# Kernel tuning notes

Hardware: AMD Instinct MI355X
Metric: run time of the kernel (lower is better)

The kernel has to match this reference:

```python
import jax, jax.numpy as jnp
import numpy as np

D_CONV = 4
D_STATE = 16
DT_RANK = 64


def _silu(x):
    return x * jax.nn.sigmoid(x)


def setup_inputs() -> dict:
    key = jax.random.key(0)
    ks = jax.random.split(key, 10)
    B, L, dim = 2, 1024, 1024
    d_inner = 2 * dim
    s = lambda fan: 1.0 / np.sqrt(fan)
    inp = {
        "x": jax.random.normal(ks[0], (B, L, dim), jnp.float32),
        "ln_w": jnp.ones((dim,), jnp.float32),
        "ln_b": jnp.zeros((dim,), jnp.float32),
        "w_in": jax.random.normal(ks[1], (2 * d_inner, dim), jnp.float32) * s(dim),
        "conv_w": jax.random.normal(ks[2], (d_inner, D_CONV), jnp.float32) * s(D_CONV),
        "conv_b": jnp.zeros((d_inner,), jnp.float32),
        "w_xproj": jax.random.normal(ks[3], (DT_RANK + 2 * D_STATE, d_inner), jnp.float32) * s(d_inner),
        "w_dt": jax.random.normal(ks[4], (d_inner, DT_RANK), jnp.float32) * s(DT_RANK),
        "b_dt": jax.random.normal(ks[5], (d_inner,), jnp.float32) * 0.1,
        # S4D-real init: A = -(1..d_state) per channel
        "a_log": jnp.tile(jnp.log(jnp.arange(1, D_STATE + 1, dtype=jnp.float32)), (d_inner, 1)),
        "d_skip": jnp.ones((d_inner,), jnp.float32),
        "w_out": jax.random.normal(ks[6], (dim, d_inner), jnp.float32) * s(d_inner),
    }
    return inp


def reference(x, ln_w, ln_b, w_in, conv_w, conv_b, w_xproj, w_dt, b_dt, a_log, d_skip, w_out):
    B, L, dim = x.shape
    residual = x

    # LayerNorm
    mu = jnp.mean(x, axis=-1, keepdims=True)
    var = jnp.mean((x - mu) ** 2, axis=-1, keepdims=True)
    xn = (x - mu) * jax.lax.rsqrt(var + 1e-5) * ln_w + ln_b

    # in_proj -> (x_ssm, z) each (B, L, d_inner)
    xz = jnp.einsum("bld,ed->ble", xn, w_in)
    d_inner = xz.shape[-1] // 2
    xs, z = xz[..., :d_inner], xz[..., d_inner:]

    # depthwise causal conv1d (kernel D_CONV) + SiLU
    xp = jnp.pad(xs, ((0, 0), (D_CONV - 1, 0), (0, 0)))
    xc = conv_b
    for k in range(D_CONV):
        xc = xc + conv_w[:, k] * xp[:, k : k + L, :]
    u = _silu(xc)  # (B, L, d_inner)

    # x_proj -> dt, B, C
    x_dbl = jnp.einsum("ble,re->blr", u, w_xproj)
    dt_r = x_dbl[..., :DT_RANK]
    B_ssm = x_dbl[..., DT_RANK : DT_RANK + D_STATE]         # (B, L, n)
    C_ssm = x_dbl[..., DT_RANK + D_STATE :]                 # (B, L, n)

    dt = jax.nn.softplus(jnp.einsum("blr,er->ble", dt_r, w_dt) + b_dt)  # (B, L, d_inner)

    A = -jnp.exp(a_log)  # (d_inner, n)
    deltaA = jnp.exp(jnp.einsum("ble,en->blen", dt, A))            # (B, L, e, n)
    deltaBu = jnp.einsum("ble,bln,ble->blen", dt, B_ssm, u)        # (B, L, e, n)

    # selective scan over L
    def step(h, ins):
        dA_t, dBu_t, C_t = ins
        h = dA_t * h + dBu_t                       # (B, e, n)
        y = jnp.einsum("ben,bn->be", h, C_t)
        return h, y

    h0 = jnp.zeros((B, d_inner, D_STATE), xs.dtype)
    _, ys = jax.lax.scan(
        step,
        h0,
        (deltaA.transpose(1, 0, 2, 3), deltaBu.transpose(1, 0, 2, 3), C_ssm.transpose(1, 0, 2)),
    )
    y = ys.transpose(1, 0, 2) + u * d_skip         # (B, L, e)

    y = y * _silu(z)
    out = jnp.einsum("ble,de->bld", y, w_out)
    return residual + out
```

## Files before the change

kernel.cpp:

```cpp
#include <hip/hip_runtime.h>
#include <hip/hip_bf16.h>


#define LC 32
#define NCHUNK 32

typedef short bf16x8 __attribute__((ext_vector_type(8)));
typedef float f32x4  __attribute__((ext_vector_type(4)));

static __device__ __forceinline__ float siluf(float x) { return x / (1.f + __expf(-x)); }
static __device__ __forceinline__ unsigned short f2bf(float f) {
    unsigned int u = __float_as_uint(f);
    unsigned int r = (u + 0x7fffu + ((u >> 16) & 1u)) >> 16;
    return (unsigned short)r;
}
static __device__ __forceinline__ float bfb(unsigned short u) {
    return __uint_as_float(((unsigned int)u) << 16);
}
static __device__ __forceinline__ void gload_lds16(const void* g, void* l) {
    __builtin_amdgcn_global_load_lds(
        (const __attribute__((address_space(1))) void*)g,
        (__attribute__((address_space(3))) void*)l, 16, 0, 0);
}

__global__ __launch_bounds__(256) void setup_kernel(
    const float* __restrict__ w_in,  unsigned short* __restrict__ w_in_b,
    const float* __restrict__ w_out, unsigned short* __restrict__ w_out_b,
    const float* __restrict__ w_dt,  unsigned short* __restrict__ w_dt_b,
    const float* __restrict__ x,
    const float* __restrict__ ln_w,
    const float* __restrict__ ln_b,
    unsigned short* __restrict__ xn)
{
    int bid = blockIdx.x, tid = threadIdx.x;
    if (bid < 6272) {
        int i = bid * 256 + tid;
        const float* in; unsigned short* outp; int j;
        if (i < 1048576)      { in = w_in;  outp = w_in_b;  j = i; }
        else if (i < 1572864) { in = w_out; outp = w_out_b; j = i - 1048576; }
        else if (i < 1605632) { in = w_dt;  outp = w_dt_b;  j = i - 1572864; }
        else return;
        float4 v = reinterpret_cast<const float4*>(in)[j];
        ushort4 o = { f2bf(v.x), f2bf(v.y), f2bf(v.z), f2bf(v.w) };
        reinterpret_cast<ushort4*>(outp)[j] = o;
        return;
    }
    int m = bid - 6272;
    const float4* xr = reinterpret_cast<const float4*>(x) + (size_t)m * 256;
    float4 r = xr[tid];
    float f0 = r.x, f1 = r.y, f2 = r.z, f3 = r.w;
    float s  = f0 + f1 + f2 + f3;
    float s2 = f0*f0 + f1*f1 + f2*f2 + f3*f3;
    #pragma unroll
    for (int off = 32; off > 0; off >>= 1) {
        s  += __shfl_down(s, off);
        s2 += __shfl_down(s2, off);
    }
    __shared__ float red[8];
    if ((tid & 63) == 0) { red[tid >> 6] = s; red[4 + (tid >> 6)] = s2; }
    __syncthreads();
    float st = red[0] + red[1] + red[2] + red[3];
    float qt = red[4] + red[5] + red[6] + red[7];
    float mu   = st * (1.f / 1024.f);
    float var  = qt * (1.f / 1024.f) - mu * mu;
    float rstd = rsqrtf(var + 1e-5f);
    float4 wv = reinterpret_cast<const float4*>(ln_w)[tid];
    float4 bv = reinterpret_cast<const float4*>(ln_b)[tid];
    ushort4 o = { f2bf((f0 - mu) * rstd * wv.x + bv.x),
                  f2bf((f1 - mu) * rstd * wv.y + bv.y),
                  f2bf((f2 - mu) * rstd * wv.z + bv.z),
                  f2bf((f3 - mu) * rstd * wv.w + bv.w) };
    reinterpret_cast<ushort4*>(xn + (size_t)m * 1024)[tid] = o;
}

__global__ __launch_bounds__(256) void gemm_bf16_nt(
    const unsigned short* __restrict__ A, int lda,
    const unsigned short* __restrict__ B, int ldb,
    int Kslice,
    float* __restrict__ C, unsigned short* __restrict__ Cb, int ldc,
    int ep, size_t Cstride)
{
    __shared__ short As[3 * 64 * 32];
    __shared__ short Bs[3 * 128 * 32];
    int tid = threadIdx.x;
    int z = blockIdx.z;
    A += (size_t)z * Kslice;
    B += (size_t)z * Kslice;
    C += (size_t)z * Cstride;

    int gx = gridDim.x;
    int wg = blockIdx.y * gx + blockIdx.x;
    int nwg = gx * gridDim.y;
    int cpx = nwg >> 3;
    int swz = (wg & 7) * cpx + (wg >> 3);
    int bx = swz % gx, by = swz / gx;

    int m0 = by * 64, n0 = bx * 128;
    int lane = tid & 63, wave = tid >> 6;
    int wm = (wave >> 1) * 32, wn = (wave & 1) * 64;
    int frow = lane & 15, fq = lane >> 4;

    f32x4 acc[2][4] = {};

    int lrow = lane >> 2;
    int scol = (lane & 3) * 8;
    const unsigned short* AgL = A + (size_t)(m0 + wave * 16 + lrow) * lda + scol;
    const unsigned short* BgL = B + (size_t)(n0 + wave * 16 + lrow) * ldb + scol;
    int aoff = (wave * 16) * 32;
    int boff = (wave * 16) * 32;

    #pragma unroll
    for (int p = 0; p < 2; ++p) {
        int nk = p * 32;
        gload_lds16(AgL + nk,                    As + p * 2048 + aoff);
        gload_lds16(BgL + nk,                    Bs + p * 4096 + boff);
        gload_lds16(BgL + (size_t)64 * ldb + nk, Bs + p * 4096 + boff + 64 * 32);
    }

    int cur = 0;
    for (int k0 = 0; k0 < Kslice; k0 += 32) {
        if (k0 + 32 < Kslice) {
            asm volatile("s_waitcnt vmcnt(3) lgkmcnt(0)" ::: "memory");
        } else {
            asm volatile("s_waitcnt vmcnt(0) lgkmcnt(0)" ::: "memory");
        }
        __builtin_amdgcn_s_barrier();
        int nk = k0 + 64;
        if (nk < Kslice) {
            int stg = cur - 1; if (stg < 0) stg = 2;
            gload_lds16(AgL + nk,                    As + stg * 2048 + aoff);
            gload_lds16(BgL + nk,                    Bs + stg * 4096 + boff);
            gload_lds16(BgL + (size_t)64 * ldb + nk, Bs + stg * 4096 + boff + 64 * 32);
        }
        const short* Ac = As + cur * 2048;
        const short* Bc = Bs + cur * 4096;
        bf16x8 af[2], bfr[4];
        #pragma unroll
        for (int i = 0; i < 2; ++i)
            af[i] = *reinterpret_cast<const bf16x8*>(Ac + (wm + i * 16 + frow) * 32 + fq * 8);
        #pragma unroll
        for (int j = 0; j < 4; ++j)
            bfr[j] = *reinterpret_cast<const bf16x8*>(Bc + (wn + j * 16 + frow) * 32 + fq * 8);
        #pragma unroll
        for (int i = 0; i < 2; ++i)
            #pragma unroll
            for (int j = 0; j < 4; ++j)
                acc[i][j] = __builtin_amdgcn_mfma_f32_16x16x32_bf16(af[i], bfr[j], acc[i][j], 0, 0, 0);
        cur = (cur == 2) ? 0 : cur + 1;
    }

    int cn = lane & 15, rq = (lane >> 4) * 4;
    #pragma unroll
    for (int i = 0; i < 2; ++i) {
        #pragma unroll
        for (int j = 0; j < 4; ++j) {
            #pragma unroll
            for (int r = 0; r < 4; ++r) {
                int row = m0 + wm + i * 16 + rq + r;
                int col = n0 + wn + j * 16 + cn;
                float v = acc[i][j][r];
                if (ep == 0) {
                    C[(size_t)row * ldc + col] = v;
                } else {
                    Cb[(size_t)row * ldc + col] = f2bf(v);
                }
            }
        }
    }
}

__global__ __launch_bounds__(256) void out_reduce(
    const float* __restrict__ part, const float* __restrict__ x,
    float* __restrict__ out)
{
    int i = blockIdx.x * 256 + threadIdx.x;
    float4 s = reinterpret_cast<const float4*>(x)[i];
    #pragma unroll
    for (int z = 0; z < 4; ++z) {
        float4 p = reinterpret_cast<const float4*>(part + (size_t)z * 2097152)[i];
        s.x += p.x; s.y += p.y; s.z += p.z; s.w += p.w;
    }
    reinterpret_cast<float4*>(out)[i] = s;
}

__global__ __launch_bounds__(256) void xproj_splitk(
    const unsigned short* __restrict__ xz,
    const float* __restrict__ cw,
    const float* __restrict__ cb,
    const float* __restrict__ B,
    unsigned short* __restrict__ u,
    float* __restrict__ part)
{
    __shared__ float As[16][68];
    __shared__ float Bs[16][100];
    int tid = threadIdx.x;
    int m0 = blockIdx.x * 64;
    int k0 = blockIdx.y * 64;
    int tx = tid & 15;
    int ty = tid >> 4;
    float acc[4][6] = {};
    int arow = tid >> 2, akg = (tid & 3) << 2;
    int brow1 = (256 + tid) >> 2, bkg1 = ((256 + tid) & 3) << 2;
    int m = m0 + arow;
    int l = m & 1023;

    for (int ks = 0; ks < 64; ks += 16) {
        int e0 = k0 + ks + akg;
        float xv[4][4];
        #pragma unroll
        for (int kk = 0; kk < 4; ++kk) {
            ushort4 t = make_ushort4(0, 0, 0, 0);
            if (l - 3 + kk >= 0)
                t = *reinterpret_cast<const ushort4*>(xz + (size_t)(m - 3 + kk) * 4096 + e0);
            xv[kk][0] = bfb(t.x); xv[kk][1] = bfb(t.y);
            xv[kk][2] = bfb(t.z); xv[kk][3] = bfb(t.w);
        }
        float4 cbv = *reinterpret_cast<const float4*>(cb + e0);
        float cbs[4] = { cbv.x, cbv.y, cbv.z, cbv.w };
        float res[4];
        #pragma unroll
        for (int j = 0; j < 4; ++j) {
            float4 w = *reinterpret_cast<const float4*>(cw + (size_t)(e0 + j) * 4);
            float a = cbs[j];
            a = fmaf(w.x, xv[0][j], a);
            a = fmaf(w.y, xv[1][j], a);
            a = fmaf(w.z, xv[2][j], a);
            a = fmaf(w.w, xv[3][j], a);
            res[j] = siluf(a);
        }
        ushort4 uo = { f2bf(res[0]), f2bf(res[1]), f2bf(res[2]), f2bf(res[3]) };
        *reinterpret_cast<ushort4*>(u + (size_t)m * 2048 + e0) = uo;

        float4 bv0 = make_float4(0.f, 0.f, 0.f, 0.f), bv1 = bv0;
        if (arow < 96)  bv0 = *reinterpret_cast<const float4*>(B + (size_t)arow * 2048 + k0 + ks + akg);
        if (brow1 < 96) bv1 = *reinterpret_cast<const float4*>(B + (size_t)brow1 * 2048 + k0 + ks + bkg1);
        __syncthreads();
        As[akg + 0][arow] = res[0]; As[akg + 1][arow] = res[1];
        As[akg + 2][arow] = res[2]; As[akg + 3][arow] = res[3];
        if (arow < 96) {
            Bs[akg + 0][arow] = bv0.x; Bs[akg + 1][arow] = bv0.y;
            Bs[akg + 2][arow] = bv0.z; Bs[akg + 3][arow] = bv0.w;
        }
        if (brow1 < 96) {
            Bs[bkg1 + 0][brow1] = bv1.x; Bs[bkg1 + 1][brow1] = bv1.y;
            Bs[bkg1 + 2][brow1] = bv1.z; Bs[bkg1 + 3][brow1] = bv1.w;
        }
        __syncthreads();
        #pragma unroll
        for (int k = 0; k < 16; ++k) {
            float aa[4], bb[6];
            #pragma unroll
            for (int i = 0; i < 4; ++i) aa[i] = As[k][ty * 4 + i];
            #pragma unroll
            for (int j = 0; j < 6; ++j) bb[j] = Bs[k][tx * 6 + j];
            #pragma unroll
            for (int i = 0; i < 4; ++i)
                #pragma unroll
                for (int j = 0; j < 6; ++j)
                    acc[i][j] = fmaf(aa[i], bb[j], acc[i][j]);
        }
    }
    float* p = part + (size_t)blockIdx.y * 196608;
    #pragma unroll
    for (int i = 0; i < 4; ++i)
        #pragma unroll
        for (int j = 0; j < 6; ++j)
            p[(size_t)(m0 + ty * 4 + i) * 96 + tx * 6 + j] = acc[i][j];
}

__global__ __launch_bounds__(256) void xproj_reduce(
    const float* __restrict__ part, float* __restrict__ xdbl)
{
    int i = blockIdx.x * 256 + threadIdx.x;
    float s = 0.f;
    #pragma unroll
    for (int sd = 0; sd < 32; ++sd) s += part[(size_t)sd * 196608 + i];
    xdbl[i] = s;
}

static __device__ __forceinline__ void dt_tile128(
    const float* __restrict__ xdbl, const unsigned short* __restrict__ w_dt_b,
    const float* __restrict__ b_dt, size_t rbase, int et,
    int lane, int wave, float dtl[LC][128])
{
    int frow = lane & 15, fq = lane >> 4;
    bf16x8 af[2][2];
    #pragma unroll
    for (int i = 0; i < 2; ++i)
        #pragma unroll
        for (int kk = 0; kk < 2; ++kk) {
            const float* ap = xdbl + (rbase + i * 16 + frow) * 96 + kk * 32 + fq * 8;
            float4 a0 = *reinterpret_cast<const float4*>(ap);
            float4 a1 = *reinterpret_cast<const float4*>(ap + 4);
            bf16x8 t;
            t[0] = (short)f2bf(a0.x); t[1] = (short)f2bf(a0.y);
            t[2] = (short)f2bf(a0.z); t[3] = (short)f2bf(a0.w);
            t[4] = (short)f2bf(a1.x); t[5] = (short)f2bf(a1.y);
            t[6] = (short)f2bf(a1.z); t[7] = (short)f2bf(a1.w);
            af[i][kk] = t;
        }
    f32x4 dacc[2][2] = {};
    #pragma unroll
    for (int j = 0; j < 2; ++j)
        #pragma unroll
        for (int kk = 0; kk < 2; ++kk) {
            int row_e = et * 128 + wave * 32 + j * 16 + frow;
            bf16x8 bfr = *reinterpret_cast<const bf16x8*>(
                w_dt_b + (size_t)row_e * 64 + kk * 32 + fq * 8);
            #pragma unroll
            for (int i = 0; i < 2; ++i)
                dacc[i][j] = __builtin_amdgcn_mfma_f32_16x16x32_bf16(af[i][kk], bfr, dacc[i][j], 0, 0, 0);
        }
    int cn = lane & 15, rq = (lane >> 4) * 4;
    #pragma unroll
    for (int i = 0; i < 2; ++i)
        #pragma unroll
        for (int j = 0; j < 2; ++j)
            #pragma unroll
            for (int r = 0; r < 4; ++r) {
                int row = i * 16 + rq + r;
                int col = wave * 32 + j * 16 + cn;
                float v = dacc[i][j][r] + b_dt[et * 128 + col];
                v = (v > 20.f) ? v : log1pf(__expf(v));
                dtl[row][col] = bfb(f2bf(v));
            }
}

__global__ __launch_bounds__(256) void scan_part1(
    const unsigned short* __restrict__ u,
    const float* __restrict__ xdbl,
    const unsigned short* __restrict__ w_dt_b,
    const float* __restrict__ b_dt,
    const float* __restrict__ a_log,
    float* __restrict__ hpart,
    float* __restrict__ Aprod)
{
    __shared__ float dtl[LC][128];
    int tid = threadIdx.x;
    int lane = tid & 63, wave = tid >> 6;
    int bid = blockIdx.x;
    int c = bid & 31, et = (bid >> 5) & 15, b = bid >> 9;
    int ch = tid >> 1, ng = tid & 1;
    int e = et * 128 + ch;
    size_t rbase = (size_t)b * 1024 + c * LC;

    dt_tile128(xdbl, w_dt_b, b_dt, rbase, et, lane, wave, dtl);

    const float L2E = 1.4426950408889634f;
    float A2[8];
    {
        float4 a0 = *reinterpret_cast<const float4*>(a_log + (size_t)e * 16 + ng * 8);
        float4 a1 = *reinterpret_cast<const float4*>(a_log + (size_t)e * 16 + ng * 8 + 4);
        A2[0] = -__expf(a0.x) * L2E; A2[1] = -__expf(a0.y) * L2E;
        A2[2] = -__expf(a0.z) * L2E; A2[3] = -__expf(a0.w) * L2E;
        A2[4] = -__expf(a1.x) * L2E; A2[5] = -__expf(a1.y) * L2E;
        A2[6] = -__expf(a1.z) * L2E; A2[7] = -__expf(a1.w) * L2E;
    }
    float h[8], P[8];
    #pragma unroll
    for (int n = 0; n < 8; ++n) { h[n] = 0.f; P[n] = 1.f; }

    const unsigned short* u_p = u + rbase * 2048 + e;
    const float* b_p = xdbl + rbase * 96 + 64 + ng * 8;
    __syncthreads();
    #pragma unroll 8
    for (int l = 0; l < LC; ++l) {
        float dtv = dtl[l][ch];
        float u_c = bfb(u_p[(size_t)l * 2048]);
        float4 b0 = *reinterpret_cast<const float4*>(b_p + (size_t)l * 96);
        float4 b1 = *reinterpret_cast<const float4*>(b_p + (size_t)l * 96 + 4);
        float Bv[8] = { b0.x, b0.y, b0.z, b0.w, b1.x, b1.y, b1.z, b1.w };
        float du = dtv * u_c;
        #pragma unroll
        for (int n = 0; n < 8; ++n) {
            float d = exp2f(dtv * A2[n]);
            h[n] = fmaf(d, h[n], du * Bv[n]);
            P[n] *= d;
        }
    }
    size_t oidx = (size_t)c * 65536 + ((size_t)b * 2048 + e) * 16 + ng * 8;
    *reinterpret_cast<float4*>(hpart + oidx)     = make_float4(h[0], h[1], h[2], h[3]);
    *reinterpret_cast<float4*>(hpart + oidx + 4) = make_float4(h[4], h[5], h[6], h[7]);
    *reinterpret_cast<float4*>(Aprod + oidx)     = make_float4(P[0], P[1], P[2], P[3]);
    *reinterpret_cast<float4*>(Aprod + oidx + 4) = make_float4(P[4], P[5], P[6], P[7]);
}

__global__ __launch_bounds__(256) void scan_combine(
    const float* __restrict__ hpart,
    const float* __restrict__ Aprod,
    float* __restrict__ hinit)
{
    int t = blockIdx.x * 256 + threadIdx.x;
    float h = 0.f;
    #pragma unroll 8
    for (int c = 0; c < NCHUNK; ++c) {
        hinit[(size_t)c * 65536 + t] = h;
        float P  = Aprod[(size_t)c * 65536 + t];
        float hp = hpart[(size_t)c * 65536 + t];
        h = fmaf(P, h, hp);
    }
}

__global__ __launch_bounds__(256) void scan_part2(
    const unsigned short* __restrict__ u,
    const float* __restrict__ xdbl,
    const unsigned short* __restrict__ w_dt_b,
    const float* __restrict__ b_dt,
    const unsigned short* __restrict__ xz,
    const float* __restrict__ a_log,
    const float* __restrict__ d_skip,
    const float* __restrict__ hinit,
    unsigned short* __restrict__ y)
{
    __shared__ float dtl[LC][128];
    int tid = threadIdx.x;
    int lane = tid & 63, wave = tid >> 6;
    int bid = blockIdx.x;
    int c = bid & 31, et = (bid >> 5) & 15, b = bid >> 9;
    int ch = tid >> 1, ng = tid & 1;
    int e = et * 128 + ch;
    size_t rbase = (size_t)b * 1024 + c * LC;

    dt_tile128(xdbl, w_dt_b, b_dt, rbase, et, lane, wave, dtl);

    const float L2E = 1.4426950408889634f;
    float A2[8];
    {
        float4 a0 = *reinterpret_cast<const float4*>(a_log + (size_t)e * 16 + ng * 8);
        float4 a1 = *reinterpret_cast<const float4*>(a_log + (size_t)e * 16 + ng * 8 + 4);
        A2[0] = -__expf(a0.x) * L2E; A2[1] = -__expf(a0.y) * L2E;
        A2[2] = -__expf(a0.z) * L2E; A2[3] = -__expf(a0.w) * L2E;
        A2[4] = -__expf(a1.x) * L2E; A2[5] = -__expf(a1.y) * L2E;
        A2[6] = -__expf(a1.z) * L2E; A2[7] = -__expf(a1.w) * L2E;
    }
    float dsk = d_skip[e];
    float h[8];
    size_t oidx = (size_t)c * 65536 + ((size_t)b * 2048 + e) * 16 + ng * 8;
    {
        float4 h0 = *reinterpret_cast<const float4*>(hinit + oidx);
        float4 h1 = *reinterpret_cast<const float4*>(hinit + oidx + 4);
        h[0] = h0.x; h[1] = h0.y; h[2] = h0.z; h[3] = h0.w;
        h[4] = h1.x; h[5] = h1.y; h[6] = h1.z; h[7] = h1.w;
    }

    const unsigned short* u_p = u + rbase * 2048 + e;
    const unsigned short* z_p = xz + rbase * 4096 + 2048 + e;
    const float* b_p = xdbl + rbase * 96 + 64 + ng * 8;
    unsigned short* y_p = y + rbase * 2048 + e;
    __syncthreads();
    #pragma unroll 8
    for (int l = 0; l < LC; ++l) {
        float dtv = dtl[l][ch];
        float u_c = bfb(u_p[(size_t)l * 2048]);
        float4 b0 = *reinterpret_cast<const float4*>(b_p + (size_t)l * 96);
        float4 b1 = *reinterpret_cast<const float4*>(b_p + (size_t)l * 96 + 4);
        float4 c0 = *reinterpret_cast<const float4*>(b_p + (size_t)l * 96 + 16);
        float4 c1 = *reinterpret_cast<const float4*>(b_p + (size_t)l * 96 + 20);
        float Bv[8] = { b0.x, b0.y, b0.z, b0.w, b1.x, b1.y, b1.z, b1.w };
        float Cv[8] = { c0.x, c0.y, c0.z, c0.w, c1.x, c1.y, c1.z, c1.w };
        float du = dtv * u_c;
        float p = 0.f;
        #pragma unroll
        for (int n = 0; n < 8; ++n) {
            float d = exp2f(dtv * A2[n]);
            h[n] = fmaf(d, h[n], du * Bv[n]);
            p = fmaf(h[n], Cv[n], p);
        }
        p += __shfl_xor(p, 1);
        if (ng == 0) {
            float zv = bfb(z_p[(size_t)l * 4096]);
            y_p[(size_t)l * 2048] = f2bf((p + u_c * dsk) * siluf(zv));
        }
    }
}

extern "C" void kernel_launch(void* const* d_in, const int* in_sizes, int n_in,
                              void* d_out, int out_size, void* d_ws, size_t ws_size,
                              hipStream_t stream) {
    const float* x       = (const float*)d_in[0];
    const float* ln_w    = (const float*)d_in[1];
    const float* ln_b    = (const float*)d_in[2];
    const float* w_in    = (const float*)d_in[3];
    const float* conv_w  = (const float*)d_in[4];
    const float* conv_b  = (const float*)d_in[5];
    const float* w_xproj = (const float*)d_in[6];
    const float* w_dt    = (const float*)d_in[7];
    const float* b_dt    = (const float*)d_in[8];
    const float* a_log   = (const float*)d_in[9];
    const float* d_skip  = (const float*)d_in[10];
    const float* w_out   = (const float*)d_in[11];
    float* out = (float*)d_out;

    float* ws = (float*)d_ws;
    unsigned short* xn_b    = (unsigned short*)(ws);
    unsigned short* xz_b    = (unsigned short*)(ws + 1048576);
    unsigned short* u_b     = (unsigned short*)(ws + 5242880);
    float* xdbl  = ws + 7340032;
    float* hpart = ws + 9633792;
    float* Aprod = ws + 13828096;
    float* hinit = ws + 18022400;
    unsigned short* y_b     = (unsigned short*)(ws + 22216704);
    unsigned short* w_in_b  = (unsigned short*)(ws + 24313856);
    unsigned short* w_out_b = (unsigned short*)(ws + 26411008);
    unsigned short* w_dt_b  = (unsigned short*)(ws + 27459584);
    float* xpart = ws + 9633792;
    float* opart = ws + 1048576;

    setup_kernel<<<8320, 256, 0, stream>>>(w_in, w_in_b, w_out, w_out_b, w_dt, w_dt_b,
                                           x, ln_w, ln_b, xn_b);
    gemm_bf16_nt<<<dim3(32, 32, 1), 256, 0, stream>>>(xn_b, 1024, w_in_b, 1024, 1024,
                                                      nullptr, xz_b, 4096, 3, 0);
    xproj_splitk<<<dim3(32, 32), 256, 0, stream>>>(xz_b, conv_w, conv_b, w_xproj,
                                                   u_b, xpart);
    xproj_reduce<<<768, 256, 0, stream>>>(xpart, xdbl);
    scan_part1<<<1024, 256, 0, stream>>>(u_b, xdbl, w_dt_b, b_dt, a_log, hpart, Aprod);
    scan_combine<<<256, 256, 0, stream>>>(hpart, Aprod, hinit);
    scan_part2<<<1024, 256, 0, stream>>>(u_b, xdbl, w_dt_b, b_dt, xz_b, a_log,
                                         d_skip, hinit, y_b);
    gemm_bf16_nt<<<dim3(8, 32, 4), 256, 0, stream>>>(y_b, 2048, w_out_b, 2048, 512,
                                                     opart, nullptr, 1024, 0, 2097152);
    out_reduce<<<2048, 256, 0, stream>>>(opart, x, out);
}
```

Before: 288.5 us.

## Halve scan chunk length, double chunk count, and stage B/C in shared memory

The chunked selective scan now uses chunks of 16 timesteps instead of 32, so there are 64 chunks and twice as many blocks in both scan passes. The dt projection tile is shrunk to match, using one MFMA row tile instead of two. The B and C vectors for each chunk are loaded once into shared memory instead of being re-read from global memory by every thread. The aim is more parallel work and shorter serial loops per block, at the cost of twice the partial-state traffic and a longer serial loop in the combine kernel.

After: 274.1 us. -5.0%, faster.

```diff
diff --git a/kernel.cpp b/kernel.cpp
--- a/kernel.cpp
+++ b/kernel.cpp
@@ -2,8 +2,8 @@
 #include <hip/hip_bf16.h>
 
 
-#define LC 32
-#define NCHUNK 32
+#define LC 16
+#define NCHUNK 64
 
 typedef short bf16x8 __attribute__((ext_vector_type(8)));
 typedef float f32x4  __attribute__((ext_vector_type(4)));
@@ -278,28 +278,26 @@
     xdbl[i] = s;
 }
 
-static __device__ __forceinline__ void dt_tile128(
+static __device__ __forceinline__ void dt_tile16(
     const float* __restrict__ xdbl, const unsigned short* __restrict__ w_dt_b,
     const float* __restrict__ b_dt, size_t rbase, int et,
     int lane, int wave, float dtl[LC][128])
 {
     int frow = lane & 15, fq = lane >> 4;
-    bf16x8 af[2][2];
-    #pragma unroll
-    for (int i = 0; i < 2; ++i)
-        #pragma unroll
-        for (int kk = 0; kk < 2; ++kk) {
-            const float* ap = xdbl + (rbase + i * 16 + frow) * 96 + kk * 32 + fq * 8;
-            float4 a0 = *reinterpret_cast<const float4*>(ap);
-            float4 a1 = *reinterpret_cast<const float4*>(ap + 4);
-            bf16x8 t;
-            t[0] = (short)f2bf(a0.x); t[1] = (short)f2bf(a0.y);
-            t[2] = (short)f2bf(a0.z); t[3] = (short)f2bf(a0.w);
-            t[4] = (short)f2bf(a1.x); t[5] = (short)f2bf(a1.y);
-            t[6] = (short)f2bf(a1.z); t[7] = (short)f2bf(a1.w);
-            af[i][kk] = t;
-        }
-    f32x4 dacc[2][2] = {};
+    bf16x8 af[2];
+    #pragma unroll
+    for (int kk = 0; kk < 2; ++kk) {
+        const float* ap = xdbl + (rbase + frow) * 96 + kk * 32 + fq * 8;
+        float4 a0 = *reinterpret_cast<const float4*>(ap);
+        float4 a1 = *reinterpret_cast<const float4*>(ap + 4);
+        bf16x8 t;
+        t[0] = (short)f2bf(a0.x); t[1] = (short)f2bf(a0.y);
+        t[2] = (short)f2bf(a0.z); t[3] = (short)f2bf(a0.w);
+        t[4] = (short)f2bf(a1.x); t[5] = (short)f2bf(a1.y);
+        t[6] = (short)f2bf(a1.z); t[7] = (short)f2bf(a1.w);
+        af[kk] = t;
+    }
+    f32x4 dacc[2] = {};
     #pragma unroll
     for (int j = 0; j < 2; ++j)
         #pragma unroll
@@ -307,23 +305,19 @@
             int row_e = et * 128 + wave * 32 + j * 16 + frow;
             bf16x8 bfr = *reinterpret_cast<const bf16x8*>(
                 w_dt_b + (size_t)row_e * 64 + kk * 32 + fq * 8);
-            #pragma unroll
-            for (int i = 0; i < 2; ++i)
-                dacc[i][j] = __builtin_amdgcn_mfma_f32_16x16x32_bf16(af[i][kk], bfr, dacc[i][j], 0, 0, 0);
+            dacc[j] = __builtin_amdgcn_mfma_f32_16x16x32_bf16(af[kk], bfr, dacc[j], 0, 0, 0);
         }
     int cn = lane & 15, rq = (lane >> 4) * 4;
     #pragma unroll
-    for (int i = 0; i < 2; ++i)
-        #pragma unroll
-        for (int j = 0; j < 2; ++j)
-            #pragma unroll
-            for (int r = 0; r < 4; ++r) {
-                int row = i * 16 + rq + r;
-                int col = wave * 32 + j * 16 + cn;
-                float v = dacc[i][j][r] + b_dt[et * 128 + col];
-                v = (v > 20.f) ? v : log1pf(__expf(v));
-                dtl[row][col] = bfb(f2bf(v));
-            }
+    for (int j = 0; j < 2; ++j)
+        #pragma unroll
+        for (int r = 0; r < 4; ++r) {
+            int row = rq + r;
+            int col = wave * 32 + j * 16 + cn;
+            float v = dacc[j][r] + b_dt[et * 128 + col];
+            v = (v > 20.f) ? v : log1pf(__expf(v));
+            dtl[row][col] = bfb(f2bf(v));
+        }
 }
 
 __global__ __launch_bounds__(256) void scan_part1(
@@ -336,15 +330,18 @@
     float* __restrict__ Aprod)
 {
     __shared__ float dtl[LC][128];
+    __shared__ float Bl[LC][16];
     int tid = threadIdx.x;
     int lane = tid & 63, wave = tid >> 6;
     int bid = blockIdx.x;
-    int c = bid & 31, et = (bid >> 5) & 15, b = bid >> 9;
+    int c = bid & 63, et = (bid >> 6) & 15, b = bid >> 10;
     int ch = tid >> 1, ng = tid & 1;
     int e = et * 128 + ch;
     size_t rbase = (size_t)b * 1024 + c * LC;
 
-    dt_tile128(xdbl, w_dt_b, b_dt, rbase, et, lane, wave, dtl);
+    Bl[tid >> 4][tid & 15] = xdbl[(rbase + (tid >> 4)) * 96 + 64 + (tid & 15)];
+
+    dt_tile16(xdbl, w_dt_b, b_dt, rbase, et, lane, wave, dtl);
 
     const float L2E = 1.4426950408889634f;
     float A2[8];
@@ -361,14 +358,13 @@
     for (int n = 0; n < 8; ++n) { h[n] = 0.f; P[n] = 1.f; }
 
     const unsigned short* u_p = u + rbase * 2048 + e;
-    const float* b_p = xdbl + rbase * 96 + 64 + ng * 8;
     __syncthreads();
     #pragma unroll 8
     for (int l = 0; l < LC; ++l) {
         float dtv = dtl[l][ch];
         float u_c = bfb(u_p[(size_t)l * 2048]);
-        float4 b0 = *reinterpret_cast<const float4*>(b_p + (size_t)l * 96);
-        float4 b1 = *reinterpret_cast<const float4*>(b_p + (size_t)l * 96 + 4);
+        float4 b0 = *reinterpret_cast<const float4*>(&Bl[l][ng * 8]);
+        float4 b1 = *reinterpret_cast<const float4*>(&Bl[l][ng * 8 + 4]);
         float Bv[8] = { b0.x, b0.y, b0.z, b0.w, b1.x, b1.y, b1.z, b1.w };
         float du = dtv * u_c;
         #pragma unroll
@@ -413,15 +409,22 @@
     unsigned short* __restrict__ y)
 {
     __shared__ float dtl[LC][128];
+    __shared__ float BCl[LC][32];
     int tid = threadIdx.x;
     int lane = tid & 63, wave = tid >> 6;
     int bid = blockIdx.x;
-    int c = bid & 31, et = (bid >> 5) & 15, b = bid >> 9;
+    int c = bid & 63, et = (bid >> 6) & 15, b = bid >> 10;
     int ch = tid >> 1, ng = tid & 1;
     int e = et * 128 + ch;
     size_t rbase = (size_t)b * 1024 + c * LC;
 
-    dt_tile128(xdbl, w_dt_b, b_dt, rbase, et, lane, wave, dtl);
+    #pragma unroll
+    for (int s = 0; s < 2; ++s) {
+        int idx = s * 256 + tid;
+        BCl[idx >> 5][idx & 31] = xdbl[(rbase + (idx >> 5)) * 96 + 64 + (idx & 31)];
+    }
+
+    dt_tile16(xdbl, w_dt_b, b_dt, rbase, et, lane, wave, dtl);
 
     const float L2E = 1.4426950408889634f;
     float A2[8];
@@ -445,17 +448,16 @@
 
     const unsigned short* u_p = u + rbase * 2048 + e;
     const unsigned short* z_p = xz + rbase * 4096 + 2048 + e;
-    const float* b_p = xdbl + rbase * 96 + 64 + ng * 8;
     unsigned short* y_p = y + rbase * 2048 + e;
     __syncthreads();
     #pragma unroll 8
     for (int l = 0; l < LC; ++l) {
         float dtv = dtl[l][ch];
         float u_c = bfb(u_p[(size_t)l * 2048]);
-        float4 b0 = *reinterpret_cast<const float4*>(b_p + (size_t)l * 96);
-        float4 b1 = *reinterpret_cast<const float4*>(b_p + (size_t)l * 96 + 4);
-        float4 c0 = *reinterpret_cast<const float4*>(b_p + (size_t)l * 96 + 16);
-        float4 c1 = *reinterpret_cast<const float4*>(b_p + (size_t)l * 96 + 20);
+        float4 b0 = *reinterpret_cast<const float4*>(&BCl[l][ng * 8]);
+        float4 b1 = *reinterpret_cast<const float4*>(&BCl[l][ng * 8 + 4]);
+        float4 c0 = *reinterpret_cast<const float4*>(&BCl[l][16 + ng * 8]);
+        float4 c1 = *reinterpret_cast<const float4*>(&BCl[l][16 + ng * 8 + 4]);
         float Bv[8] = { b0.x, b0.y, b0.z, b0.w, b1.x, b1.y, b1.z, b1.w };
         float Cv[8] = { c0.x, c0.y, c0.z, c0.w, c1.x, c1.y, c1.z, c1.w };
         float du = dtv * u_c;
@@ -513,9 +515,9 @@
     xproj_splitk<<<dim3(32, 32), 256, 0, stream>>>(xz_b, conv_w, conv_b, w_xproj,
                                                    u_b, xpart);
     xproj_reduce<<<768, 256, 0, stream>>>(xpart, xdbl);
-    scan_part1<<<1024, 256, 0, stream>>>(u_b, xdbl, w_dt_b, b_dt, a_log, hpart, Aprod);
+    scan_part1<<<2048, 256, 0, stream>>>(u_b, xdbl, w_dt_b, b_dt, a_log, hpart, Aprod);
     scan_combine<<<256, 256, 0, stream>>>(hpart, Aprod, hinit);
-    scan_part2<<<1024, 256, 0, stream>>>(u_b, xdbl, w_dt_b, b_dt, xz_b, a_log,
+    scan_part2<<<2048, 256, 0, stream>>>(u_b, xdbl, w_dt_b, b_dt, xz_b, a_log,
                                          d_skip, hinit, y_b);
     gemm_bf16_nt<<<dim3(8, 32, 4), 256, 0, stream>>>(y_b, 2048, w_out_b, 2048, 512,
                                                      opart, nullptr, 1024, 0, 2097152);
```
